# Optimization experiments

Measured on AMD Instinct MI355X. Metric: run time of the kernel, lower is better.

The kernel has to match this reference:

```python
import jax, jax.numpy as jnp
import numpy as np

N = 16384
E = 262144
IN_F, HID, ENC = 3, 128, 768
NEG_SLOPE = 0.2
EPS = 1e-5


def _glorot(key, shape):
    lim = float(np.sqrt(6.0 / (shape[0] + shape[1])))
    return jax.random.uniform(key, shape, jnp.float32, -lim, lim)


def layernorm(x, g, b):
    mu = jnp.mean(x, axis=-1, keepdims=True)
    var = jnp.mean(jnp.square(x - mu), axis=-1, keepdims=True)
    return (x - mu) * jax.lax.rsqrt(var + EPS) * g + b


def gatv2(x, src, dst, Wl, bl, Wr, br, att, bias, n_nodes):
    # single-head GATv2: message = lin_l(x)[src], score from lin_l(x)[src] + lin_r(x)[dst]
    xl = x @ Wl + bl                                  # [N, C]
    xr = x @ Wr + br                                  # [N, C]
    e = jax.nn.leaky_relu(xl[src] + xr[dst], NEG_SLOPE) @ att   # [E]
    m = jax.ops.segment_max(e, dst, num_segments=n_nodes)       # per-dst max (self-loops => no empty segs)
    ex = jnp.exp(e - m[dst])
    denom = jax.ops.segment_sum(ex, dst, num_segments=n_nodes)
    alpha = ex / denom[dst]                           # [E]
    out = jax.ops.segment_sum(alpha[:, None] * xl[src], dst, num_segments=n_nodes)
    return out + bias


def setup_inputs() -> dict:
    key = jax.random.key(0)
    ks = jax.random.split(key, 12)
    x = jax.random.normal(ks[0], (N, IN_F), jnp.float32)
    edge_index = jax.random.randint(ks[1], (2, E), 0, N, jnp.int64)
    return {
        "x": x,
        "edge_index": edge_index,
        "Wfc": _glorot(ks[2], (IN_F, ENC)),
        "bfc": jnp.zeros((ENC,), jnp.float32),
        "W1l": _glorot(ks[3], (IN_F, HID)),
        "b1l": jnp.zeros((HID,), jnp.float32),
        "W1r": _glorot(ks[4], (IN_F, HID)),
        "b1r": jnp.zeros((HID,), jnp.float32),
        "att1": _glorot(ks[5], (HID, 1))[:, 0],
        "bias1": jnp.zeros((HID,), jnp.float32),
        "g_bn1": jnp.ones((HID,), jnp.float32),
        "bb_bn1": jnp.zeros((HID,), jnp.float32),
        "W2l": _glorot(ks[6], (HID, ENC)),
        "b2l": jnp.zeros((ENC,), jnp.float32),
        "W2r": _glorot(ks[7], (HID, ENC)),
        "b2r": jnp.zeros((ENC,), jnp.float32),
        "att2": _glorot(ks[8], (ENC, 1))[:, 0],
        "bias2": jnp.zeros((ENC,), jnp.float32),
        "g_norm": jnp.ones((ENC,), jnp.float32),
        "b_norm": jnp.zeros((ENC,), jnp.float32),
    }


def reference(x, edge_index, Wfc, bfc, W1l, b1l, W1r, b1r, att1, bias1,
              g_bn1, bb_bn1, W2l, b2l, W2r, b2r, att2, bias2, g_norm, b_norm):
    loops = jnp.arange(N, dtype=edge_index.dtype)
    src = jnp.concatenate([edge_index[0], loops])   # add self-loops (PyG default)
    dst = jnp.concatenate([edge_index[1], loops])
    res = x @ Wfc + bfc                              # [N, ENC]
    h = gatv2(x, src, dst, W1l, b1l, W1r, b1r, att1, bias1, N)
    h = jax.nn.elu(layernorm(h, g_bn1, bb_bn1))
    h = gatv2(h, src, dst, W2l, b2l, W2r, b2r, att2, bias2, N)
    return layernorm(h + res, g_norm, b_norm)
```

## Files before the change

### kernel.cpp

```cpp
#include <hip/hip_runtime.h>

#define N_NODES 16384
#define N_EDGES 262144
#define EP (N_EDGES + N_NODES)
#define HID 128
#define ENC 768
#define EPSV 1e-5f

typedef unsigned short u16;
typedef unsigned char u8;
using f32x4  = __attribute__((ext_vector_type(4))) float;
using bf16x8 = __attribute__((ext_vector_type(8))) short;
using v2f    = __attribute__((ext_vector_type(2))) float;

__device__ __forceinline__ float wave_sum(float v){
  #pragma unroll
  for(int m=32;m>=1;m>>=1) v += __shfl_xor(v, m, 64);
  return v;
}
__device__ __forceinline__ unsigned bf16rtne(float f){
  const unsigned u = __float_as_uint(f);
  return (u + 0x7fffu + ((u>>16)&1u)) >> 16;
}
__device__ __forceinline__ unsigned pack2(float a, float b){
  return bf16rtne(a) | (bf16rtne(b) << 16);
}
__device__ __forceinline__ float bf2f(u16 h){ return __uint_as_float(((unsigned)h) << 16); }
__device__ __forceinline__ float plo(unsigned u){ return __uint_as_float(u << 16); }
__device__ __forceinline__ float phi(unsigned u){ return __uint_as_float(u & 0xffff0000u); }
__device__ __forceinline__ u8 f2fp8(float v){
  return (u8)(__builtin_amdgcn_cvt_pk_fp8_f32(v, v, 0, false) & 0xff);
}

#define Q4(ax, j, q) { \
  const v2f f01 = __builtin_amdgcn_cvt_pk_f32_fp8(ax, false); \
  const v2f f23 = __builtin_amdgcn_cvt_pk_f32_fp8(ax, true);  \
  q = fmaf(sg[j],   __builtin_fabsf(f01.x+xr[j]),   q); \
  q = fmaf(sg[j+1], __builtin_fabsf(f01.y+xr[j+1]), q); \
  q = fmaf(sg[j+2], __builtin_fabsf(f23.x+xr[j+2]), q); \
  q = fmaf(sg[j+3], __builtin_fabsf(f23.y+xr[j+3]), q); }

#define LIN1_BLKS (N_NODES/4)
#define WPREP_BLKS (2*ENC*HID/256)
#define HIST_BLKS (EP/256)
#define W2A_BLKS 258
__global__ __launch_bounds__(256) void prep_kernel(
    const float* __restrict__ x,
    const float* __restrict__ W1l, const float* __restrict__ b1l,
    const float* __restrict__ W1r, const float* __restrict__ b1r,
    const float* __restrict__ att1,
    const float* __restrict__ W2l, const float* __restrict__ W2r,
    const float* __restrict__ b2l, const float* __restrict__ b2r,
    const float* __restrict__ att2,
    const int* __restrict__ ei,
    unsigned* __restrict__ xl1u, unsigned* __restrict__ xr1u,
    float* __restrict__ dotl1, float* __restrict__ dotr1,
    u16* __restrict__ Wtb, float* __restrict__ w2a,
    int* __restrict__ hist){
  const int bid = blockIdx.x;
  if(bid < LIN1_BLKS){
    const int lane = threadIdx.x & 63;
    const int n = bid*4 + (threadIdx.x >> 6);
    const float x0 = x[n*3], x1 = x[n*3+1], x2 = x[n*3+2];
    const int c0 = 2*lane, c1 = 2*lane + 1;
    const float la = x0*W1l[c0] + x1*W1l[HID+c0] + x2*W1l[2*HID+c0] + b1l[c0];
    const float lb = x0*W1l[c1] + x1*W1l[HID+c1] + x2*W1l[2*HID+c1] + b1l[c1];
    const float ra = x0*W1r[c0] + x1*W1r[HID+c0] + x2*W1r[2*HID+c0] + b1r[c0];
    const float rb = x0*W1r[c1] + x1*W1r[HID+c1] + x2*W1r[2*HID+c1] + b1r[c1];
    const float aa = att1[c0], ab = att1[c1];
    const float dl = wave_sum(la*aa + lb*ab);
    const float dr = wave_sum(ra*aa + rb*ab);
    if(lane == 0){ dotl1[n] = 0.6f*dl; dotr1[n] = 0.6f*dr; }
    xl1u[n*64+lane] = pack2(la, lb);
    xr1u[n*64+lane] = pack2(ra, rb);
  } else if(bid < LIN1_BLKS + WPREP_BLKS){
    const int idx = (bid - LIN1_BLKS)*256 + threadIdx.x;
    const int n = idx >> 7, k = idx & 127;
    const float v = (n < ENC) ? W2l[k*ENC + n] : W2r[k*ENC + (n-ENC)];
    Wtb[idx] = (u16)bf16rtne(v);
  } else if(bid < LIN1_BLKS + WPREP_BLKS + HIST_BLKS){
    const int i = (bid - LIN1_BLKS - WPREP_BLKS)*256 + threadIdx.x;
    const int dst = (i < N_EDGES) ? ei[N_EDGES + i] : (i - N_EDGES);
    atomicAdd(&hist[dst], 1);
  } else {
    const int idx = bid - (LIN1_BLKS + WPREP_BLKS + HIST_BLKS);
    const float* src = (idx < 128) ? (W2l + (size_t)idx*ENC)
                     : (idx < 256) ? (W2r + (size_t)(idx-128)*ENC)
                     : (idx == 256) ? b2l : b2r;
    float partial = 0.f;
    for(int c = threadIdx.x; c < ENC; c += 256) partial += src[c]*att2[c];
    partial = wave_sum(partial);
    __shared__ float red4[4];
    if((threadIdx.x & 63) == 0) red4[threadIdx.x >> 6] = partial;
    __syncthreads();
    if(threadIdx.x == 0) w2a[idx] = red4[0]+red4[1]+red4[2]+red4[3];
  }
}

__global__ __launch_bounds__(1024) void scan_kernel(
    const int* __restrict__ hist, int* __restrict__ rowstart){
  __shared__ int sums[1024];
  const int t = threadIdx.x;
  const int base = t*16;
  int loc[16];
  int s = 0;
  #pragma unroll
  for(int i=0;i<16;i++){ loc[i] = s; s += hist[base+i]; }
  sums[t] = s;
  __syncthreads();
  for(int off=1; off<1024; off<<=1){
    int v = 0;
    if(t >= off) v = sums[t-off];
    __syncthreads();
    if(t >= off) sums[t] += v;
    __syncthreads();
  }
  const int prev = (t==0) ? 0 : sums[t-1];
  #pragma unroll
  for(int i=0;i<16;i++) rowstart[base+i] = prev + loc[i];
  if(t == 1023) rowstart[N_NODES] = EP;
}

__global__ __launch_bounds__(256) void scatter_kernel(
    const int* __restrict__ ei, const int* __restrict__ rowstart,
    int* __restrict__ cursor, int* __restrict__ ssrc){
  const int i = blockIdx.x*256 + threadIdx.x;
  const int src = (i < N_EDGES) ? ei[i]           : (i - N_EDGES);
  const int dst = (i < N_EDGES) ? ei[N_EDGES + i] : (i - N_EDGES);
  const int pos = rowstart[dst] + atomicAdd(&cursor[dst], 1);
  ssrc[pos] = src;
}

__global__ __launch_bounds__(256) void node1_kernel(
    const unsigned* __restrict__ xl1u, const unsigned* __restrict__ xr1u,
    const float* __restrict__ att1,
    const float* __restrict__ dotl1, const float* __restrict__ dotr1,
    const float* __restrict__ bias1,
    const float* __restrict__ g1, const float* __restrict__ b1,
    const float* __restrict__ w2a,
    const int* __restrict__ rowstart, const int* __restrict__ ssrc,
    unsigned* __restrict__ h1u,
    float* __restrict__ dotl2, float* __restrict__ dotr2){
  const int lane = threadIdx.x & 63;
  const int n = blockIdx.x*4 + (threadIdx.x >> 6);
  const int g = lane >> 4, k = lane & 15;
  float xr[8], sa[8];
  {
    const uint4 u = *(const uint4*)(xr1u + n*64 + 4*k);
    xr[0]=plo(u.x); xr[1]=phi(u.x); xr[2]=plo(u.y); xr[3]=phi(u.y);
    xr[4]=plo(u.z); xr[5]=phi(u.z); xr[6]=plo(u.w); xr[7]=phi(u.w);
    const float4 a0 = *(const float4*)(att1 + 8*k);
    const float4 a1 = *(const float4*)(att1 + 8*k + 4);
    sa[0]=0.4f*a0.x; sa[1]=0.4f*a0.y; sa[2]=0.4f*a0.z; sa[3]=0.4f*a0.w;
    sa[4]=0.4f*a1.x; sa[5]=0.4f*a1.y; sa[6]=0.4f*a1.z; sa[7]=0.4f*a1.w;
  }
  const float ebase = dotr1[n];
  float acc[8] = {0,0,0,0,0,0,0,0};
  float denom = 0.f;
  const int p0 = rowstart[n], p1 = rowstart[n+1];
  for(int base = p0; base < p1; base += 4){
    const int idx = base + g;
    const bool valid = idx < p1;
    const int s = ssrc[valid ? idx : (p1-1)];
    const uint4 u = *(const uint4*)(xl1u + s*64 + 4*k);
    float a[8];
    a[0]=plo(u.x); a[1]=phi(u.x); a[2]=plo(u.y); a[3]=phi(u.y);
    a[4]=plo(u.z); a[5]=phi(u.z); a[6]=plo(u.w); a[7]=phi(u.w);
    const float dlv = dotl1[s];
    float q = 0.f;
    #pragma unroll
    for(int j=0;j<8;j++) q = fmaf(sa[j], __builtin_fabsf(a[j]+xr[j]), q);
    q += __shfl_xor(q, 1, 64);
    q += __shfl_xor(q, 2, 64);
    q += __shfl_xor(q, 4, 64);
    q += __shfl_xor(q, 8, 64);
    float w = __expf(q + dlv + ebase);
    w = valid ? w : 0.f;
    denom += w;
    #pragma unroll
    for(int j=0;j<8;j++) acc[j] = fmaf(w, a[j], acc[j]);
  }
  #pragma unroll
  for(int m=16; m<64; m<<=1){
    denom += __shfl_xor(denom, m, 64);
    #pragma unroll
    for(int j=0;j<8;j++) acc[j] += __shfl_xor(acc[j], m, 64);
  }
  const float inv = 1.f/denom;
  const float4 bb0 = *(const float4*)(bias1 + 8*k);
  const float4 bb1 = *(const float4*)(bias1 + 8*k + 4);
  float y[8];
  y[0]=acc[0]*inv+bb0.x; y[1]=acc[1]*inv+bb0.y; y[2]=acc[2]*inv+bb0.z; y[3]=acc[3]*inv+bb0.w;
  y[4]=acc[4]*inv+bb1.x; y[5]=acc[5]*inv+bb1.y; y[6]=acc[6]*inv+bb1.z; y[7]=acc[7]*inv+bb1.w;
  float ls = 0.f, lq = 0.f;
  #pragma unroll
  for(int j=0;j<8;j++){ ls += y[j]; lq += y[j]*y[j]; }
  ls = wave_sum(ls); lq = wave_sum(lq);
  const float mu  = ls * (1.f/(4*HID));
  const float var = lq * (1.f/(4*HID)) - mu*mu;
  const float r = rsqrtf(var + EPSV);
  const float4 gg0 = *(const float4*)(g1 + 8*k);
  const float4 gg1 = *(const float4*)(g1 + 8*k + 4);
  const float4 ob0 = *(const float4*)(b1 + 8*k);
  const float4 ob1 = *(const float4*)(b1 + 8*k + 4);
  const float gv[8] = {gg0.x,gg0.y,gg0.z,gg0.w,gg1.x,gg1.y,gg1.z,gg1.w};
  const float bv[8] = {ob0.x,ob0.y,ob0.z,ob0.w,ob1.x,ob1.y,ob1.z,ob1.w};
  float z[8];
  #pragma unroll
  for(int j=0;j<8;j++){
    float zz = (y[j]-mu)*r*gv[j] + bv[j];
    z[j] = zz > 0.f ? zz : expm1f(zz);
  }
  float dl2 = 0.f, dr2 = 0.f;
  #pragma unroll
  for(int j=0;j<8;j++){
    dl2 = fmaf(z[j], w2a[8*k+j], dl2);
    dr2 = fmaf(z[j], w2a[128+8*k+j], dr2);
  }
  dl2 = wave_sum(dl2); dr2 = wave_sum(dr2);
  if(lane == 0){
    dotl2[n] = 0.6f*(0.25f*dl2 + w2a[256]);
    dotr2[n] = 0.6f*(0.25f*dr2 + w2a[257]);
  }
  if(g == 0){
    uint4 o;
    o.x = pack2(z[0], z[1]); o.y = pack2(z[2], z[3]);
    o.z = pack2(z[4], z[5]); o.w = pack2(z[6], z[7]);
    *(uint4*)(h1u + n*64 + 4*k) = o;
  }
}

#define LBM 128
#define LBN 128
__global__ __launch_bounds__(256) void mfma_lin2_kernel(
    const u16* __restrict__ h1b, const u16* __restrict__ Wtb,
    const float* __restrict__ b2l, const float* __restrict__ b2r,
    u8* __restrict__ xl8, u16* __restrict__ xr2u){
  __shared__ __align__(16) u16 Cs[LBM*128];
  const int t = threadIdx.x;
  const int mb = blockIdx.x * LBM;
  const int nb = blockIdx.y * LBN;
  const int w = t >> 6, lane = t & 63;
  const int l15 = lane & 15, g = lane >> 4;
  const int ar0 = mb + w*32 + l15, ar1 = ar0 + 16;
  bf16x8 a0[4], a1[4];
  #pragma unroll
  for(int ks=0;ks<4;ks++){
    a0[ks] = *(const bf16x8*)(h1b + (size_t)ar0*128 + ks*32 + g*8);
    a1[ks] = *(const bf16x8*)(h1b + (size_t)ar1*128 + ks*32 + g*8);
  }
  f32x4 acc0[8], acc1[8];
  #pragma unroll
  for(int j=0;j<8;j++){ acc0[j]=(f32x4){0,0,0,0}; acc1[j]=(f32x4){0,0,0,0}; }
  #pragma unroll
  for(int j=0;j<8;j++){
    const int brn = nb + j*16 + l15;
    #pragma unroll
    for(int ks=0;ks<4;ks++){
      const bf16x8 b = *(const bf16x8*)(Wtb + (size_t)brn*128 + ks*32 + g*8);
      acc0[j] = __builtin_amdgcn_mfma_f32_16x16x32_bf16(a0[ks], b, acc0[j], 0,0,0);
      acc1[j] = __builtin_amdgcn_mfma_f32_16x16x32_bf16(a1[ks], b, acc1[j], 0,0,0);
    }
  }
  if(nb < ENC){
    u8* Cs8 = (u8*)Cs;
    float biasj[8];
    #pragma unroll
    for(int j=0;j<8;j++) biasj[j] = b2l[nb + j*16 + l15];
    #pragma unroll
    for(int j=0;j<8;j++){
      const int col = j*16 + l15;
      #pragma unroll
      for(int r4=0;r4<4;r4++){
        const int row0 = w*32 + g*4 + r4;
        Cs8[row0*128 + (col ^ ((row0&7)<<4))] = f2fp8(acc0[j][r4] + biasj[j]);
        const int row1 = row0 + 16;
        Cs8[row1*128 + (col ^ ((row1&7)<<4))] = f2fp8(acc1[j][r4] + biasj[j]);
      }
    }
    __syncthreads();
    #pragma unroll
    for(int idx=t; idx<LBM*8; idx+=256){
      const int row = idx >> 3, ch = idx & 7;
      const uint4 v = *(const uint4*)(Cs8 + row*128 + ((ch*16) ^ ((row&7)<<4)));
      *(uint4*)(xl8 + (size_t)(mb+row)*ENC + nb + ch*16) = v;
    }
  } else {
    const float* bsrc = b2r + (nb - ENC);
    float biasj[8];
    #pragma unroll
    for(int j=0;j<8;j++) biasj[j] = bsrc[j*16 + l15];
    #pragma unroll
    for(int j=0;j<8;j++){
      const int coll = j*16 + l15;
      #pragma unroll
      for(int r4=0;r4<4;r4++){
        const int row0 = w*32 + g*4 + r4;
        *(u16*)((char*)Cs + row0*256 + ((coll*2) ^ ((row0&7)<<4))) =
            (u16)bf16rtne(acc0[j][r4] + biasj[j]);
        const int row1 = row0 + 16;
        *(u16*)((char*)Cs + row1*256 + ((coll*2) ^ ((row1&7)<<4))) =
            (u16)bf16rtne(acc1[j][r4] + biasj[j]);
      }
    }
    __syncthreads();
    u16* dst0 = xr2u + (nb - ENC);
    const int rr = t >> 4, cc = t & 15;
    #pragma unroll
    for(int it=0; it<8; ++it){
      const int row = it*16 + rr;
      const uint4 v = *(const uint4*)((const char*)Cs + row*256 + ((cc*16) ^ ((row&7)<<4)));
      *(uint4*)(dst0 + (size_t)(mb+row)*ENC + cc*8) = v;
    }
  }
}

__global__ __launch_bounds__(256) void node2b_kernel(
    const u8* __restrict__ xl8, const u8* __restrict__ xr2u8,
    const float* __restrict__ att2,
    const float* __restrict__ dotl2, const float* __restrict__ dotr2,
    const unsigned* __restrict__ h1u,
    const int* __restrict__ rowstart, const int* __restrict__ ssrc,
    unsigned* __restrict__ aggb){
  __shared__ float comb[4][64][4];
  const int lane = threadIdx.x & 63;
  const int wid = threadIdx.x >> 6;
  const int n = blockIdx.x*2 + (wid >> 1);
  const int half = wid & 1;
  float sg[12], xr[12];
  {
    const float4* A4 = (const float4*)(att2 + lane*12);
    const float4 s0 = A4[0], s1 = A4[1], s2 = A4[2];
    sg[0]=0.4f*s0.x; sg[1]=0.4f*s0.y; sg[2]=0.4f*s0.z; sg[3]=0.4f*s0.w;
    sg[4]=0.4f*s1.x; sg[5]=0.4f*s1.y; sg[6]=0.4f*s1.z; sg[7]=0.4f*s1.w;
    sg[8]=0.4f*s2.x; sg[9]=0.4f*s2.y; sg[10]=0.4f*s2.z; sg[11]=0.4f*s2.w;
    const u8* xrrow = xr2u8 + (size_t)n*(ENC*2) + lane*24;
    const uint2 r0 = *(const uint2*)(xrrow);
    const uint2 r1 = *(const uint2*)(xrrow + 8);
    const uint2 r2 = *(const uint2*)(xrrow + 16);
    xr[0]=plo(r0.x); xr[1]=phi(r0.x); xr[2]=plo(r0.y); xr[3]=phi(r0.y);
    xr[4]=plo(r1.x); xr[5]=phi(r1.x); xr[6]=plo(r1.y); xr[7]=phi(r1.y);
    xr[8]=plo(r2.x); xr[9]=phi(r2.x); xr[10]=plo(r2.y); xr[11]=phi(r2.y);
  }
  const float ebase = dotr2[n];
  float denom = 0.f, acc0 = 0.f, acc1 = 0.f;
  const int p0 = rowstart[n], p1v = rowstart[n+1];
  const int mid = p0 + ((p1v - p0 + 1) >> 1);
  int p = half ? mid : p0;
  const int pe = half ? p1v : mid;
  for(; p+3 < pe; p += 4){
    const int s0 = ssrc[p],   s1 = ssrc[p+1];
    const int s2 = ssrc[p+2], s3 = ssrc[p+3];
    const uint3 a0 = *(const uint3*)(xl8 + (size_t)s0*ENC + lane*12);
    const uint3 a1 = *(const uint3*)(xl8 + (size_t)s1*ENC + lane*12);
    const uint3 a2 = *(const uint3*)(xl8 + (size_t)s2*ENC + lane*12);
    const uint3 a3 = *(const uint3*)(xl8 + (size_t)s3*ENC + lane*12);
    const float dl0 = dotl2[s0], dl1 = dotl2[s1];
    const float dl2 = dotl2[s2], dl3 = dotl2[s3];
    const unsigned h0 = h1u[s0*64 + lane];
    const unsigned h1 = h1u[s1*64 + lane];
    const unsigned h2 = h1u[s2*64 + lane];
    const unsigned h3 = h1u[s3*64 + lane];
    float q0 = 0.f, q1 = 0.f, q2 = 0.f, q3 = 0.f;
    Q4(a0.x, 0, q0) Q4(a0.y, 4, q0) Q4(a0.z, 8, q0)
    Q4(a1.x, 0, q1) Q4(a1.y, 4, q1) Q4(a1.z, 8, q1)
    Q4(a2.x, 0, q2) Q4(a2.y, 4, q2) Q4(a2.z, 8, q2)
    Q4(a3.x, 0, q3) Q4(a3.y, 4, q3) Q4(a3.z, 8, q3)
    #pragma unroll
    for(int m=32;m>=1;m>>=1){
      q0 += __shfl_xor(q0, m, 64);
      q1 += __shfl_xor(q1, m, 64);
      q2 += __shfl_xor(q2, m, 64);
      q3 += __shfl_xor(q3, m, 64);
    }
    const float w0 = __expf(q0 + dl0 + ebase), w1 = __expf(q1 + dl1 + ebase);
    const float w2 = __expf(q2 + dl2 + ebase), w3 = __expf(q3 + dl3 + ebase);
    denom += (w0+w1) + (w2+w3);
    acc0 += w0*plo(h0) + w1*plo(h1) + w2*plo(h2) + w3*plo(h3);
    acc1 += w0*phi(h0) + w1*phi(h1) + w2*phi(h2) + w3*phi(h3);
  }
  for(; p < pe; ++p){
    const int s0 = ssrc[p];
    const uint3 a0 = *(const uint3*)(xl8 + (size_t)s0*ENC + lane*12);
    float q0 = 0.f;
    Q4(a0.x, 0, q0) Q4(a0.y, 4, q0) Q4(a0.z, 8, q0)
    const unsigned h0 = h1u[s0*64 + lane];
    const float w0 = __expf(wave_sum(q0) + dotl2[s0] + ebase);
    denom += w0; acc0 += w0*plo(h0); acc1 += w0*phi(h0);
  }
  comb[wid][lane][0] = denom;
  comb[wid][lane][1] = acc0;
  comb[wid][lane][2] = acc1;
  __syncthreads();
  if(half == 0){
    denom += comb[wid+1][lane][0];
    acc0  += comb[wid+1][lane][1];
    acc1  += comb[wid+1][lane][2];
    const float inv = 1.f/denom;
    aggb[n*64 + lane] = pack2(acc0*inv, acc1*inv);
  }
}

#define YSTR 770
__global__ __launch_bounds__(256) void gemm3_mfma_kernel(
    const u16* __restrict__ aggb, const u16* __restrict__ Wtb,
    const float* __restrict__ b2l, const float* __restrict__ bias2,
    const float* __restrict__ x, const float* __restrict__ Wfc,
    const float* __restrict__ bfc,
    const float* __restrict__ gn, const float* __restrict__ bn,
    float* __restrict__ out){
  __shared__ u16 Ys[64*YSTR];
  __shared__ float cbs[ENC];
  __shared__ float wfs[3][ENC];
  __shared__ float mus[64], rss[64];
  const int t = threadIdx.x;
  const int mb = blockIdx.x * 64;
  for(int c=t; c<ENC; c+=256){
    cbs[c] = b2l[c] + bias2[c] + bfc[c];
    wfs[0][c] = Wfc[c]; wfs[1][c] = Wfc[ENC+c]; wfs[2][c] = Wfc[2*ENC+c];
  }
  const int w = t >> 6, lane = t & 63;
  const int l15 = lane & 15, g = lane >> 4;
  const int ar = mb + w*16 + l15;
  bf16x8 a[4];
  #pragma unroll
  for(int ks=0;ks<4;ks++)
    a[ks] = *(const bf16x8*)(aggb + (size_t)ar*128 + ks*32 + g*8);
  float xv0[4], xv1[4], xv2[4];
  #pragma unroll
  for(int r4=0;r4<4;r4++){
    const int rrow = mb + w*16 + g*4 + r4;
    xv0[r4] = x[rrow*3]; xv1[r4] = x[rrow*3+1]; xv2[r4] = x[rrow*3+2];
  }
  float rs[4] = {0,0,0,0}, rq[4] = {0,0,0,0};
  __syncthreads();
  #pragma unroll
  for(int sub=0; sub<6; ++sub){
    const int nb = sub*128;
    f32x4 acc[8];
    #pragma unroll
    for(int j=0;j<8;j++) acc[j]=(f32x4){0,0,0,0};
    #pragma unroll
    for(int j=0;j<8;j++){
      const int brn = nb + j*16 + l15;
      #pragma unroll
      for(int ks=0;ks<4;ks++){
        const bf16x8 b = *(const bf16x8*)(Wtb + (size_t)brn*128 + ks*32 + g*8);
        acc[j] = __builtin_amdgcn_mfma_f32_16x16x32_bf16(a[ks], b, acc[j], 0,0,0);
      }
    }
    #pragma unroll
    for(int j=0;j<8;j++){
      const int col = nb + j*16 + l15;
      const float cb = cbs[col];
      const float w0 = wfs[0][col], w1 = wfs[1][col], w2 = wfs[2][col];
      #pragma unroll
      for(int r4=0;r4<4;r4++){
        const int lrow = w*16 + g*4 + r4;
        const float y = acc[j][r4] + cb + xv0[r4]*w0 + xv1[r4]*w1 + xv2[r4]*w2;
        rs[r4] += y; rq[r4] += y*y;
        Ys[lrow*YSTR + col] = (u16)bf16rtne(y);
      }
    }
  }
  #pragma unroll
  for(int m=8;m>=1;m>>=1){
    #pragma unroll
    for(int r4=0;r4<4;r4++){
      rs[r4] += __shfl_xor(rs[r4], m, 64);
      rq[r4] += __shfl_xor(rq[r4], m, 64);
    }
  }
  if(l15 == 0){
    #pragma unroll
    for(int r4=0;r4<4;r4++){
      const int lrow = w*16 + g*4 + r4;
      const float mu = rs[r4] * (1.f/ENC);
      const float var = rq[r4] * (1.f/ENC) - mu*mu;
      mus[lrow] = mu;
      rss[lrow] = rsqrtf(var + EPSV);
    }
  }
  __syncthreads();
  float gv[12], bv[12];
  #pragma unroll
  for(int j2=0;j2<12;j2++){ gv[j2] = gn[lane + j2*64]; bv[j2] = bn[lane + j2*64]; }
  for(int r=0; r<16; ++r){
    const int lrow = w*16 + r;
    const float mu = mus[lrow], rstd = rss[lrow];
    float* orow = out + (size_t)(mb+lrow)*ENC;
    #pragma unroll
    for(int j2=0;j2<12;j2++){
      const float y = bf2f(Ys[lrow*YSTR + lane + j2*64]);
      orow[lane + j2*64] = (y - mu)*rstd*gv[j2] + bv[j2];
    }
  }
}

extern "C" void kernel_launch(void* const* d_in, const int* in_sizes, int n_in,
                              void* d_out, int out_size, void* d_ws, size_t ws_size,
                              hipStream_t stream) {
  const float* x    = (const float*)d_in[0];
  const int*   ei   = (const int*)  d_in[1];
  const float* Wfc  = (const float*)d_in[2];
  const float* bfc  = (const float*)d_in[3];
  const float* W1l  = (const float*)d_in[4];
  const float* b1l  = (const float*)d_in[5];
  const float* W1r  = (const float*)d_in[6];
  const float* b1r  = (const float*)d_in[7];
  const float* att1 = (const float*)d_in[8];
  const float* bias1= (const float*)d_in[9];
  const float* g1   = (const float*)d_in[10];
  const float* bb1  = (const float*)d_in[11];
  const float* W2l  = (const float*)d_in[12];
  const float* b2l  = (const float*)d_in[13];
  const float* W2r  = (const float*)d_in[14];
  const float* b2r  = (const float*)d_in[15];
  const float* att2 = (const float*)d_in[16];
  const float* bias2= (const float*)d_in[17];
  const float* gn   = (const float*)d_in[18];
  const float* bn   = (const float*)d_in[19];
  float* out = (float*)d_out;

  char* w = (char*)d_ws;
  auto alloc = [&](size_t bytes){ void* p = (void*)w; w += (bytes + 255) & ~(size_t)255; return p; };
  int*      hist     = (int*)     alloc((size_t)N_NODES*4);
  int*      cursor   = (int*)     alloc((size_t)N_NODES*4);
  int*      rowstart = (int*)     alloc((size_t)(N_NODES+1)*4);
  int*      ssrc     = (int*)     alloc((size_t)EP*4);
  unsigned* xl1u     = (unsigned*)alloc((size_t)N_NODES*64*4);
  unsigned* xr1u     = (unsigned*)alloc((size_t)N_NODES*64*4);
  float*    dotl1    = (float*)   alloc((size_t)N_NODES*4);
  float*    dotr1    = (float*)   alloc((size_t)N_NODES*4);
  float*    dotl2    = (float*)   alloc((size_t)N_NODES*4);
  float*    dotr2    = (float*)   alloc((size_t)N_NODES*4);
  unsigned* h1u      = (unsigned*)alloc((size_t)N_NODES*64*4);
  unsigned* aggb     = (unsigned*)alloc((size_t)N_NODES*64*4);
  u8*       xl8      = (u8*)      alloc((size_t)N_NODES*ENC);
  u16*      xr2u     = (u16*)     alloc((size_t)N_NODES*ENC*2);
  u16*      Wtb      = (u16*)     alloc((size_t)2*ENC*HID*2);
  float*    w2a      = (float*)   alloc((size_t)W2A_BLKS*4);

  hipMemsetAsync(hist, 0, (size_t)N_NODES*8, stream);

  prep_kernel<<<LIN1_BLKS+WPREP_BLKS+HIST_BLKS+W2A_BLKS, 256, 0, stream>>>(
      x, W1l, b1l, W1r, b1r, att1, W2l, W2r, b2l, b2r, att2, ei,
      xl1u, xr1u, dotl1, dotr1, Wtb, w2a, hist);
  scan_kernel<<<1, 1024, 0, stream>>>(hist, rowstart);
  scatter_kernel<<<EP/256, 256, 0, stream>>>(ei, rowstart, cursor, ssrc);
  node1_kernel<<<N_NODES/4, 256, 0, stream>>>(xl1u, xr1u, att1, dotl1, dotr1,
                                              bias1, g1, bb1, w2a,
                                              rowstart, ssrc, h1u, dotl2, dotr2);
  mfma_lin2_kernel<<<dim3(N_NODES/LBM, 2*ENC/LBN), 256, 0, stream>>>(
      (const u16*)h1u, Wtb, b2l, b2r, xl8, xr2u);
  node2b_kernel<<<N_NODES/2, 256, 0, stream>>>(xl8, (const u8*)xr2u, att2,
                                               dotl2, dotr2, h1u,
                                               rowstart, ssrc, aggb);
  gemm3_mfma_kernel<<<N_NODES/64, 256, 0, stream>>>((const u16*)aggb, Wtb, b2l, bias2,
                                                    x, Wfc, bfc, gn, bn, out);
}
```

Measured before the change: 191.7 us.

## Process two edges per wave with half-wave groups in GATv2 layer-2 aggregation

```diff
diff --git a/kernel.cpp b/kernel.cpp
--- a/kernel.cpp
+++ b/kernel.cpp
@@ -18,6 +18,11 @@
   for(int m=32;m>=1;m>>=1) v += __shfl_xor(v, m, 64);
   return v;
 }
+__device__ __forceinline__ float g32_sum(float v){
+  #pragma unroll
+  for(int m=16;m>=1;m>>=1) v += __shfl_xor(v, m, 64);
+  return v;
+}
 __device__ __forceinline__ unsigned bf16rtne(float f){
   const unsigned u = __float_as_uint(f);
   return (u + 0x7fffu + ((u>>16)&1u)) >> 16;
@@ -32,7 +37,7 @@
   return (u8)(__builtin_amdgcn_cvt_pk_fp8_f32(v, v, 0, false) & 0xff);
 }
 
-#define Q4(ax, j, q) { \
+#define QD(ax, j, q) { \
   const v2f f01 = __builtin_amdgcn_cvt_pk_f32_fp8(ax, false); \
   const v2f f23 = __builtin_amdgcn_cvt_pk_f32_fp8(ax, true);  \
   q = fmaf(sg[j],   __builtin_fabsf(f01.x+xr[j]),   q); \
@@ -322,82 +327,89 @@
     const unsigned* __restrict__ h1u,
     const int* __restrict__ rowstart, const int* __restrict__ ssrc,
     unsigned* __restrict__ aggb){
-  __shared__ float comb[4][64][4];
   const int lane = threadIdx.x & 63;
-  const int wid = threadIdx.x >> 6;
-  const int n = blockIdx.x*2 + (wid >> 1);
-  const int half = wid & 1;
-  float sg[12], xr[12];
+  const int n = blockIdx.x*4 + (threadIdx.x >> 6);
+  const int g = lane >> 5, k = lane & 31;
+  float sg[24], xr[24];
+  #pragma unroll
+  for(int j4=0;j4<6;j4++){
+    const float4 s = *(const float4*)(att2 + 24*k + 4*j4);
+    sg[4*j4]=0.4f*s.x; sg[4*j4+1]=0.4f*s.y; sg[4*j4+2]=0.4f*s.z; sg[4*j4+3]=0.4f*s.w;
+  }
   {
-    const float4* A4 = (const float4*)(att2 + lane*12);
-    const float4 s0 = A4[0], s1 = A4[1], s2 = A4[2];
-    sg[0]=0.4f*s0.x; sg[1]=0.4f*s0.y; sg[2]=0.4f*s0.z; sg[3]=0.4f*s0.w;
-    sg[4]=0.4f*s1.x; sg[5]=0.4f*s1.y; sg[6]=0.4f*s1.z; sg[7]=0.4f*s1.w;
-    sg[8]=0.4f*s2.x; sg[9]=0.4f*s2.y; sg[10]=0.4f*s2.z; sg[11]=0.4f*s2.w;
-    const u8* xrrow = xr2u8 + (size_t)n*(ENC*2) + lane*24;
-    const uint2 r0 = *(const uint2*)(xrrow);
-    const uint2 r1 = *(const uint2*)(xrrow + 8);
-    const uint2 r2 = *(const uint2*)(xrrow + 16);
-    xr[0]=plo(r0.x); xr[1]=phi(r0.x); xr[2]=plo(r0.y); xr[3]=phi(r0.y);
-    xr[4]=plo(r1.x); xr[5]=phi(r1.x); xr[6]=plo(r1.y); xr[7]=phi(r1.y);
-    xr[8]=plo(r2.x); xr[9]=phi(r2.x); xr[10]=plo(r2.y); xr[11]=phi(r2.y);
+    const u8* xrrow = xr2u8 + (size_t)n*(ENC*2) + 48*k;
+    #pragma unroll
+    for(int j=0;j<3;j++){
+      const uint4 r = *(const uint4*)(xrrow + 16*j);
+      xr[8*j]  =plo(r.x); xr[8*j+1]=phi(r.x); xr[8*j+2]=plo(r.y); xr[8*j+3]=phi(r.y);
+      xr[8*j+4]=plo(r.z); xr[8*j+5]=phi(r.z); xr[8*j+6]=plo(r.w); xr[8*j+7]=phi(r.w);
+    }
   }
   const float ebase = dotr2[n];
-  float denom = 0.f, acc0 = 0.f, acc1 = 0.f;
-  const int p0 = rowstart[n], p1v = rowstart[n+1];
-  const int mid = p0 + ((p1v - p0 + 1) >> 1);
-  int p = half ? mid : p0;
-  const int pe = half ? p1v : mid;
-  for(; p+3 < pe; p += 4){
-    const int s0 = ssrc[p],   s1 = ssrc[p+1];
-    const int s2 = ssrc[p+2], s3 = ssrc[p+3];
-    const uint3 a0 = *(const uint3*)(xl8 + (size_t)s0*ENC + lane*12);
-    const uint3 a1 = *(const uint3*)(xl8 + (size_t)s1*ENC + lane*12);
-    const uint3 a2 = *(const uint3*)(xl8 + (size_t)s2*ENC + lane*12);
-    const uint3 a3 = *(const uint3*)(xl8 + (size_t)s3*ENC + lane*12);
-    const float dl0 = dotl2[s0], dl1 = dotl2[s1];
-    const float dl2 = dotl2[s2], dl3 = dotl2[s3];
-    const unsigned h0 = h1u[s0*64 + lane];
-    const unsigned h1 = h1u[s1*64 + lane];
-    const unsigned h2 = h1u[s2*64 + lane];
-    const unsigned h3 = h1u[s3*64 + lane];
-    float q0 = 0.f, q1 = 0.f, q2 = 0.f, q3 = 0.f;
-    Q4(a0.x, 0, q0) Q4(a0.y, 4, q0) Q4(a0.z, 8, q0)
-    Q4(a1.x, 0, q1) Q4(a1.y, 4, q1) Q4(a1.z, 8, q1)
-    Q4(a2.x, 0, q2) Q4(a2.y, 4, q2) Q4(a2.z, 8, q2)
-    Q4(a3.x, 0, q3) Q4(a3.y, 4, q3) Q4(a3.z, 8, q3)
-    #pragma unroll
-    for(int m=32;m>=1;m>>=1){
-      q0 += __shfl_xor(q0, m, 64);
-      q1 += __shfl_xor(q1, m, 64);
-      q2 += __shfl_xor(q2, m, 64);
-      q3 += __shfl_xor(q3, m, 64);
-    }
-    const float w0 = __expf(q0 + dl0 + ebase), w1 = __expf(q1 + dl1 + ebase);
-    const float w2 = __expf(q2 + dl2 + ebase), w3 = __expf(q3 + dl3 + ebase);
-    denom += (w0+w1) + (w2+w3);
-    acc0 += w0*plo(h0) + w1*plo(h1) + w2*plo(h2) + w3*plo(h3);
-    acc1 += w0*phi(h0) + w1*phi(h1) + w2*phi(h2) + w3*phi(h3);
-  }
-  for(; p < pe; ++p){
-    const int s0 = ssrc[p];
-    const uint3 a0 = *(const uint3*)(xl8 + (size_t)s0*ENC + lane*12);
-    float q0 = 0.f;
-    Q4(a0.x, 0, q0) Q4(a0.y, 4, q0) Q4(a0.z, 8, q0)
-    const unsigned h0 = h1u[s0*64 + lane];
-    const float w0 = __expf(wave_sum(q0) + dotl2[s0] + ebase);
-    denom += w0; acc0 += w0*plo(h0); acc1 += w0*phi(h0);
-  }
-  comb[wid][lane][0] = denom;
-  comb[wid][lane][1] = acc0;
-  comb[wid][lane][2] = acc1;
-  __syncthreads();
-  if(half == 0){
-    denom += comb[wid+1][lane][0];
-    acc0  += comb[wid+1][lane][1];
-    acc1  += comb[wid+1][lane][2];
+  float denom = 0.f, acc0 = 0.f, acc1 = 0.f, acc2 = 0.f, acc3 = 0.f;
+  const int p0 = rowstart[n], p1 = rowstart[n+1];
+  int p = p0;
+  for(; p+3 < p1; p += 4){
+    const int sA = ssrc[p + g];
+    const int sB = ssrc[p + 2 + g];
+    const u8* rA = xl8 + (size_t)sA*ENC + 24*k;
+    const u8* rB = xl8 + (size_t)sB*ENC + 24*k;
+    const uint2 xA0 = *(const uint2*)(rA);
+    const uint2 xA1 = *(const uint2*)(rA + 8);
+    const uint2 xA2 = *(const uint2*)(rA + 16);
+    const uint2 xB0 = *(const uint2*)(rB);
+    const uint2 xB1 = *(const uint2*)(rB + 8);
+    const uint2 xB2 = *(const uint2*)(rB + 16);
+    const uint2 hA = *(const uint2*)(h1u + sA*64 + 2*k);
+    const uint2 hB = *(const uint2*)(h1u + sB*64 + 2*k);
+    const float dlA = dotl2[sA], dlB = dotl2[sB];
+    float qA = 0.f, qB = 0.f;
+    QD(xA0.x, 0, qA) QD(xA0.y, 4, qA) QD(xA1.x, 8, qA)
+    QD(xA1.y, 12, qA) QD(xA2.x, 16, qA) QD(xA2.y, 20, qA)
+    QD(xB0.x, 0, qB) QD(xB0.y, 4, qB) QD(xB1.x, 8, qB)
+    QD(xB1.y, 12, qB) QD(xB2.x, 16, qB) QD(xB2.y, 20, qB)
+    #pragma unroll
+    for(int m=16;m>=1;m>>=1){
+      qA += __shfl_xor(qA, m, 64);
+      qB += __shfl_xor(qB, m, 64);
+    }
+    const float wA = __expf(qA + dlA + ebase);
+    const float wB = __expf(qB + dlB + ebase);
+    denom += wA + wB;
+    acc0 += wA*plo(hA.x) + wB*plo(hB.x);
+    acc1 += wA*phi(hA.x) + wB*phi(hB.x);
+    acc2 += wA*plo(hA.y) + wB*plo(hB.y);
+    acc3 += wA*phi(hA.y) + wB*phi(hB.y);
+  }
+  for(; p < p1; p += 2){
+    const int idx = p + g;
+    const bool valid = idx < p1;
+    const int s = ssrc[valid ? idx : p];
+    const u8* r = xl8 + (size_t)s*ENC + 24*k;
+    const uint2 x0 = *(const uint2*)(r);
+    const uint2 x1 = *(const uint2*)(r + 8);
+    const uint2 x2 = *(const uint2*)(r + 16);
+    const uint2 h = *(const uint2*)(h1u + s*64 + 2*k);
+    const float dl = dotl2[s];
+    float q = 0.f;
+    QD(x0.x, 0, q) QD(x0.y, 4, q) QD(x1.x, 8, q)
+    QD(x1.y, 12, q) QD(x2.x, 16, q) QD(x2.y, 20, q)
+    q = g32_sum(q);
+    float w = __expf(q + dl + ebase);
+    w = valid ? w : 0.f;
+    denom += w;
+    acc0 += w*plo(h.x); acc1 += w*phi(h.x);
+    acc2 += w*plo(h.y); acc3 += w*phi(h.y);
+  }
+  denom += __shfl_xor(denom, 32, 64);
+  acc0 += __shfl_xor(acc0, 32, 64);
+  acc1 += __shfl_xor(acc1, 32, 64);
+  acc2 += __shfl_xor(acc2, 32, 64);
+  acc3 += __shfl_xor(acc3, 32, 64);
+  if(g == 0){
     const float inv = 1.f/denom;
-    aggb[n*64 + lane] = pack2(acc0*inv, acc1*inv);
+    aggb[n*64 + 2*k]     = pack2(acc0*inv, acc1*inv);
+    aggb[n*64 + 2*k + 1] = pack2(acc2*inv, acc3*inv);
   }
 }
 
@@ -553,7 +565,7 @@
                                               rowstart, ssrc, h1u, dotl2, dotr2);
   mfma_lin2_kernel<<<dim3(N_NODES/LBM, 2*ENC/LBN), 256, 0, stream>>>(
       (const u16*)h1u, Wtb, b2l, b2r, xl8, xr2u);
-  node2b_kernel<<<N_NODES/2, 256, 0, stream>>>(xl8, (const u8*)xr2u, att2,
+  node2b_kernel<<<N_NODES/4, 256, 0, stream>>>(xl8, (const u8*)xr2u, att2,
                                                dotl2, dotr2, h1u,
                                                rowstart, ssrc, aggb);
   gemm3_mfma_kernel<<<N_NODES/64, 256, 0, stream>>>((const u16*)aggb, Wtb, b2l, bias2,
```

Measured after the change: 202.5 us. +5.6%, slower.
